# Performance work log

Hardware: AMD Instinct MI355X
Metric: run time of the kernel (lower is better)

Reference implementation:

```python
import jax, jax.numpy as jnp
import numpy as np

B, T, D = 32, 4096, 512  # D = 2 * hidden_size


def setup_inputs() -> dict:
    key = jax.random.key(0)
    k_h, k_w1, k_b1, k_w2 = jax.random.split(key, 4)
    scale = 1.0 / np.sqrt(D)
    return {
        "hidden_states": jax.random.normal(k_h, (B, T, D), dtype=jnp.float32),
        "W1": jax.random.normal(k_w1, (D, D), dtype=jnp.float32) * scale,
        "b1": jax.random.normal(k_b1, (D,), dtype=jnp.float32) * scale,
        "W2": jax.random.normal(k_w2, (D, D), dtype=jnp.float32) * scale,
    }


def reference(hidden_states, W1, b1, W2):
    # u = tanh(h @ W1^T + b1)        [B, T, D]
    u = jnp.tanh(jnp.einsum("btd,ed->bte", hidden_states, W1) + b1)
    # alphas = softmax over time axis of u @ W2^T (no bias)   [B, T, D]
    alphas = jax.nn.softmax(jnp.einsum("btd,ed->bte", u, W2), axis=1)
    # Original loop cats weighted [T, D] slices along dim 0 then sums dim 0,
    # i.e. a global reduction over batch AND time -> [D]
    return jnp.sum(hidden_states * alphas, axis=(0, 1))
```

## Files before the change

kernel.cpp:

```cpp
#include <hip/hip_runtime.h>
#include <math.h>

#define BATCH 32
#define TLEN  4096
#define DDIM  512
#define BM    128
#define BLOCK 512

typedef __attribute__((ext_vector_type(8)))  short bf16x8;
typedef __attribute__((ext_vector_type(16))) float f32x16;
typedef __attribute__((ext_vector_type(4)))  short s16x4;

__device__ __forceinline__ short f32_to_bf16_rne(float f) {
    union { float f; unsigned int u; } v; v.f = f;
    unsigned int r = (v.u + 0x7FFFu + ((v.u >> 16) & 1u)) >> 16;
    return (short)r;
}
__device__ __forceinline__ float fast_tanh(float x) {
    x = fminf(fmaxf(x, -15.f), 15.f);
    float t = __expf(2.0f * x);
    return (t - 1.0f) / (t + 1.0f);
}

__device__ __forceinline__ int lds_idx(int r, int c) {
    int g = (c >> 3) ^ (r & 31);
    return r * DDIM + (g << 3) + (c & 7);
}

__global__ void prep_kernel(const float* __restrict__ W1, const float* __restrict__ W2,
                            short* __restrict__ W1pk, short* __restrict__ W2pk,
                            float* __restrict__ lbuf, float* __restrict__ gbuf) {
    int i = blockIdx.x * blockDim.x + threadIdx.x;
    int e  = i >> 6;
    int d0 = (i & 63) << 3;
    int E = e >> 5, r = e & 31, C = d0 >> 4, half = (d0 >> 3) & 1;
    size_t src = (size_t)e * DDIM + d0;
    size_t dst = ((size_t)(E * 32 + C) * 64 + half * 32 + r) * 8;
    bf16x8 p1, p2;
    #pragma unroll
    for (int j = 0; j < 8; ++j) {
        p1[j] = f32_to_bf16_rne(W1[src + j]);
        p2[j] = f32_to_bf16_rne(W2[src + j]);
    }
    *(bf16x8*)&W1pk[dst] = p1;
    *(bf16x8*)&W2pk[dst] = p2;
    if (i < BATCH * DDIM) { lbuf[i] = 0.f; gbuf[i] = 0.f; }
}

__global__ __launch_bounds__(BLOCK, 2)
void main_kernel(const float* __restrict__ h,
                 const short* __restrict__ W1pk,
                 const float* __restrict__ b1,
                 const short* __restrict__ W2pk,
                 float* __restrict__ lbuf, float* __restrict__ gbuf) {
    __shared__ __align__(16) short sh[BM * DDIM];

    const int tid  = threadIdx.x;
    const int row0 = blockIdx.x * BM;
    const int b    = row0 / TLEN;

    {
        const float4* hp = (const float4*)(h + (size_t)row0 * DDIM);
        #pragma unroll
        for (int i = 0; i < (BM * DDIM / 4) / BLOCK; ++i) {
            int idx  = tid + i * BLOCK;
            float4 v = hp[idx];
            int flat = idx * 4;
            int r = flat >> 9;
            int c = flat & (DDIM - 1);
            s16x4 p;
            p.x = f32_to_bf16_rne(v.x); p.y = f32_to_bf16_rne(v.y);
            p.z = f32_to_bf16_rne(v.z); p.w = f32_to_bf16_rne(v.w);
            *(s16x4*)&sh[lds_idx(r, c)] = p;
        }
    }
    __syncthreads();

    const int wave = tid >> 6;
    const int lane = tid & 63;
    const int l32  = lane & 31;
    const int h5   = lane >> 5;
    const int e0   = wave * 64;

    f32x16 acc[2][4];
    #pragma unroll
    for (int i = 0; i < 2; ++i)
        #pragma unroll
        for (int j = 0; j < 4; ++j)
            #pragma unroll
            for (int r = 0; r < 16; ++r) acc[i][j][r] = 0.f;

    const short* W1p = W1pk + (size_t)(e0 >> 5) * (32 * 512) + lane * 8;
    bf16x8 wc[2][2], wn[2][2];
    #pragma unroll
    for (int eb = 0; eb < 2; ++eb)
        #pragma unroll
        for (int ks = 0; ks < 2; ++ks)
            wc[eb][ks] = *(const bf16x8*)(W1p + (eb * 32 + ks) * 512);

    #pragma unroll
    for (int i = 0; i < 16; ++i) {
        const int k0 = i * 32;
        bf16x8 hf[4][2];
        #pragma unroll
        for (int tb = 0; tb < 4; ++tb)
            #pragma unroll
            for (int ks = 0; ks < 2; ++ks)
                hf[tb][ks] = *(const bf16x8*)&sh[lds_idx(tb * 32 + l32,
                                                         k0 + ks * 16 + 8 * h5)];
        if (i < 15) {
            #pragma unroll
            for (int eb = 0; eb < 2; ++eb)
                #pragma unroll
                for (int ks = 0; ks < 2; ++ks)
                    wn[eb][ks] = *(const bf16x8*)(W1p + (eb * 32 + 2 * (i + 1) + ks) * 512);
        }
        #pragma unroll
        for (int eb = 0; eb < 2; ++eb)
            #pragma unroll
            for (int tb = 0; tb < 4; ++tb)
                #pragma unroll
                for (int ks = 0; ks < 2; ++ks)
                    acc[eb][tb] = __builtin_amdgcn_mfma_f32_32x32x16_bf16(
                        wc[eb][ks], hf[tb][ks], acc[eb][tb], 0, 0, 0);
        #pragma unroll
        for (int eb = 0; eb < 2; ++eb)
            #pragma unroll
            for (int ks = 0; ks < 2; ++ks) wc[eb][ks] = wn[eb][ks];
    }

    const short* W2p = W2pk + (size_t)(e0 >> 5) * (32 * 512) + lane * 8;
    bf16x8 w2c[2][2], w2n[2][2];
    #pragma unroll
    for (int cb = 0; cb < 2; ++cb)
        #pragma unroll
        for (int ks = 0; ks < 2; ++ks)
            w2c[cb][ks] = *(const bf16x8*)(W2p + (cb * 32 + ks) * 512);

    #pragma unroll
    for (int eb = 0; eb < 2; ++eb) {
        float4 bv[4];
        #pragma unroll
        for (int q = 0; q < 4; ++q)
            bv[q] = *(const float4*)&b1[e0 + 32 * eb + 4 * h5 + 8 * q];
        #pragma unroll
        for (int tb = 0; tb < 4; ++tb)
            #pragma unroll
            for (int r = 0; r < 16; ++r)
                acc[eb][tb][r] = fast_tanh(acc[eb][tb][r] + bv[r >> 2][r & 3]);
    }

    __syncthreads();

    #pragma unroll
    for (int eb = 0; eb < 2; ++eb)
        #pragma unroll
        for (int tb = 0; tb < 4; ++tb) {
            int tt = tb * 32 + l32;
            #pragma unroll
            for (int q = 0; q < 4; ++q) {
                int e = e0 + 32 * eb + 4 * h5 + 8 * q;
                s16x4 p;
                p.x = f32_to_bf16_rne(acc[eb][tb][4 * q + 0]);
                p.y = f32_to_bf16_rne(acc[eb][tb][4 * q + 1]);
                p.z = f32_to_bf16_rne(acc[eb][tb][4 * q + 2]);
                p.w = f32_to_bf16_rne(acc[eb][tb][4 * q + 3]);
                *(s16x4*)&sh[lds_idx(tt, e)] = p;
            }
        }
    __syncthreads();

    f32x16 acc2[4][2];
    #pragma unroll
    for (int i = 0; i < 4; ++i)
        #pragma unroll
        for (int j = 0; j < 2; ++j)
            #pragma unroll
            for (int r = 0; r < 16; ++r) acc2[i][j][r] = 0.f;

    #pragma unroll
    for (int i = 0; i < 16; ++i) {
        const int k0 = i * 32;
        bf16x8 uf[4][2];
        #pragma unroll
        for (int tb = 0; tb < 4; ++tb)
            #pragma unroll
            for (int ks = 0; ks < 2; ++ks)
                uf[tb][ks] = *(const bf16x8*)&sh[lds_idx(tb * 32 + l32,
                                                         k0 + ks * 16 + 8 * h5)];
        if (i < 15) {
            #pragma unroll
            for (int cb = 0; cb < 2; ++cb)
                #pragma unroll
                for (int ks = 0; ks < 2; ++ks)
                    w2n[cb][ks] = *(const bf16x8*)(W2p + (cb * 32 + 2 * (i + 1) + ks) * 512);
        }
        #pragma unroll
        for (int tb = 0; tb < 4; ++tb)
            #pragma unroll
            for (int cb = 0; cb < 2; ++cb)
                #pragma unroll
                for (int ks = 0; ks < 2; ++ks)
                    acc2[tb][cb] = __builtin_amdgcn_mfma_f32_32x32x16_bf16(
                        uf[tb][ks], w2c[cb][ks], acc2[tb][cb], 0, 0, 0);
        #pragma unroll
        for (int cb = 0; cb < 2; ++cb)
            #pragma unroll
            for (int ks = 0; ks < 2; ++ks) w2c[cb][ks] = w2n[cb][ks];
    }

    #pragma unroll
    for (int cb = 0; cb < 2; ++cb) {
        const int e2 = e0 + 32 * cb + l32;
        const float* hp2 = h + (size_t)row0 * DDIM + e2;
        float lsum = 0.f, gsum = 0.f;
        #pragma unroll
        for (int tb = 0; tb < 4; ++tb)
            #pragma unroll
            for (int r = 0; r < 16; ++r) {
                int tt = tb * 32 + 4 * h5 + (r & 3) + 8 * (r >> 2);
                float ev = __expf(acc2[tb][cb][r]);
                lsum += ev;
                gsum += ev * hp2[(size_t)tt * DDIM];
            }
        lsum += __shfl_xor(lsum, 32);
        gsum += __shfl_xor(gsum, 32);
        if (h5 == 0) {
            atomicAdd(&lbuf[b * DDIM + e2], lsum);
            atomicAdd(&gbuf[b * DDIM + e2], gsum);
        }
    }
}

__global__ void finish_kernel(const float* __restrict__ lbuf,
                              const float* __restrict__ gbuf,
                              float* __restrict__ out) {
    int d = blockIdx.x * blockDim.x + threadIdx.x;
    float s = 0.f;
    #pragma unroll
    for (int b = 0; b < BATCH; ++b)
        s += gbuf[b * DDIM + d] / lbuf[b * DDIM + d];
    out[d] = s;
}

extern "C" void kernel_launch(void* const* d_in, const int* in_sizes, int n_in,
                              void* d_out, int out_size, void* d_ws, size_t ws_size,
                              hipStream_t stream) {
    const float* h  = (const float*)d_in[0];
    const float* W1 = (const float*)d_in[1];
    const float* b1 = (const float*)d_in[2];
    const float* W2 = (const float*)d_in[3];
    float* out = (float*)d_out;

    char* ws = (char*)d_ws;
    short* W1pk = (short*)ws;
    short* W2pk = (short*)(ws + 512 * 1024);
    float* lbuf = (float*)(ws + 1024 * 1024);
    float* gbuf = (float*)(ws + 1024 * 1024 + 64 * 1024);

    prep_kernel<<<128, 256, 0, stream>>>(W1, W2, W1pk, W2pk, lbuf, gbuf);
    main_kernel<<<(BATCH * TLEN) / BM, BLOCK, 0, stream>>>(h, W1pk, b1, W2pk, lbuf, gbuf);
    finish_kernel<<<2, 256, 0, stream>>>(lbuf, gbuf, out);
}
```

Baseline: 563.8 us.

## Double block to 1024 threads with each wave covering 32 output columns

Each workgroup now runs 16 waves instead of 8, and each wave computes a 32-column slice of both GEMMs instead of 64. This halves per-wave accumulator and weight registers and doubles the waves per CU, since the 128KB LDS tile allows only one block per CU. The cost is that each wave reads the full h/u tile from LDS for half the MFMA work, doubling LDS read traffic per MFMA. The launch bounds now request 4 blocks per CU, which may constrain register allocation.

```diff
diff --git a/kernel.cpp b/kernel.cpp
--- a/kernel.cpp
+++ b/kernel.cpp
@@ -5,7 +5,7 @@
 #define TLEN  4096
 #define DDIM  512
 #define BM    128
-#define BLOCK 512
+#define BLOCK 1024
 
 typedef __attribute__((ext_vector_type(8)))  short bf16x8;
 typedef __attribute__((ext_vector_type(16))) float f32x16;
@@ -47,7 +47,7 @@
     if (i < BATCH * DDIM) { lbuf[i] = 0.f; gbuf[i] = 0.f; }
 }
 
-__global__ __launch_bounds__(BLOCK, 2)
+__global__ __launch_bounds__(BLOCK, 4)
 void main_kernel(const float* __restrict__ h,
                  const short* __restrict__ W1pk,
                  const float* __restrict__ b1,
@@ -80,23 +80,19 @@
     const int lane = tid & 63;
     const int l32  = lane & 31;
     const int h5   = lane >> 5;
-    const int e0   = wave * 64;
-
-    f32x16 acc[2][4];
-    #pragma unroll
-    for (int i = 0; i < 2; ++i)
-        #pragma unroll
-        for (int j = 0; j < 4; ++j)
-            #pragma unroll
-            for (int r = 0; r < 16; ++r) acc[i][j][r] = 0.f;
-
-    const short* W1p = W1pk + (size_t)(e0 >> 5) * (32 * 512) + lane * 8;
-    bf16x8 wc[2][2], wn[2][2];
-    #pragma unroll
-    for (int eb = 0; eb < 2; ++eb)
-        #pragma unroll
-        for (int ks = 0; ks < 2; ++ks)
-            wc[eb][ks] = *(const bf16x8*)(W1p + (eb * 32 + ks) * 512);
+    const int e0   = wave * 32;
+
+    f32x16 acc[4];
+    #pragma unroll
+    for (int j = 0; j < 4; ++j)
+        #pragma unroll
+        for (int r = 0; r < 16; ++r) acc[j][r] = 0.f;
+
+    const short* W1p = W1pk + (size_t)wave * (32 * 512) + lane * 8;
+    bf16x8 wc[2], wn[2];
+    #pragma unroll
+    for (int ks = 0; ks < 2; ++ks)
+        wc[ks] = *(const bf16x8*)(W1p + ks * 512);
 
     #pragma unroll
     for (int i = 0; i < 16; ++i) {
@@ -110,73 +106,60 @@
                                                          k0 + ks * 16 + 8 * h5)];
         if (i < 15) {
             #pragma unroll
-            for (int eb = 0; eb < 2; ++eb)
-                #pragma unroll
-                for (int ks = 0; ks < 2; ++ks)
-                    wn[eb][ks] = *(const bf16x8*)(W1p + (eb * 32 + 2 * (i + 1) + ks) * 512);
-        }
-        #pragma unroll
-        for (int eb = 0; eb < 2; ++eb)
-            #pragma unroll
-            for (int tb = 0; tb < 4; ++tb)
-                #pragma unroll
-                for (int ks = 0; ks < 2; ++ks)
-                    acc[eb][tb] = __builtin_amdgcn_mfma_f32_32x32x16_bf16(
-                        wc[eb][ks], hf[tb][ks], acc[eb][tb], 0, 0, 0);
-        #pragma unroll
-        for (int eb = 0; eb < 2; ++eb)
-            #pragma unroll
-            for (int ks = 0; ks < 2; ++ks) wc[eb][ks] = wn[eb][ks];
-    }
-
-    const short* W2p = W2pk + (size_t)(e0 >> 5) * (32 * 512) + lane * 8;
-    bf16x8 w2c[2][2], w2n[2][2];
-    #pragma unroll
-    for (int cb = 0; cb < 2; ++cb)
-        #pragma unroll
-        for (int ks = 0; ks < 2; ++ks)
-            w2c[cb][ks] = *(const bf16x8*)(W2p + (cb * 32 + ks) * 512);
-
-    #pragma unroll
-    for (int eb = 0; eb < 2; ++eb) {
+            for (int ks = 0; ks < 2; ++ks)
+                wn[ks] = *(const bf16x8*)(W1p + (2 * (i + 1) + ks) * 512);
+        }
+        #pragma unroll
+        for (int tb = 0; tb < 4; ++tb)
+            #pragma unroll
+            for (int ks = 0; ks < 2; ++ks)
+                acc[tb] = __builtin_amdgcn_mfma_f32_32x32x16_bf16(
+                    wc[ks], hf[tb][ks], acc[tb], 0, 0, 0);
+        #pragma unroll
+        for (int ks = 0; ks < 2; ++ks) wc[ks] = wn[ks];
+    }
+
+    const short* W2p = W2pk + (size_t)wave * (32 * 512) + lane * 8;
+    bf16x8 w2c[2], w2n[2];
+    #pragma unroll
+    for (int ks = 0; ks < 2; ++ks)
+        w2c[ks] = *(const bf16x8*)(W2p + ks * 512);
+
+    {
         float4 bv[4];
         #pragma unroll
         for (int q = 0; q < 4; ++q)
-            bv[q] = *(const float4*)&b1[e0 + 32 * eb + 4 * h5 + 8 * q];
+            bv[q] = *(const float4*)&b1[e0 + 4 * h5 + 8 * q];
         #pragma unroll
         for (int tb = 0; tb < 4; ++tb)
             #pragma unroll
             for (int r = 0; r < 16; ++r)
-                acc[eb][tb][r] = fast_tanh(acc[eb][tb][r] + bv[r >> 2][r & 3]);
+                acc[tb][r] = fast_tanh(acc[tb][r] + bv[r >> 2][r & 3]);
     }
 
     __syncthreads();
 
     #pragma unroll
-    for (int eb = 0; eb < 2; ++eb)
-        #pragma unroll
-        for (int tb = 0; tb < 4; ++tb) {
-            int tt = tb * 32 + l32;
-            #pragma unroll
-            for (int q = 0; q < 4; ++q) {
-                int e = e0 + 32 * eb + 4 * h5 + 8 * q;
-                s16x4 p;
-                p.x = f32_to_bf16_rne(acc[eb][tb][4 * q + 0]);
-                p.y = f32_to_bf16_rne(acc[eb][tb][4 * q + 1]);
-                p.z = f32_to_bf16_rne(acc[eb][tb][4 * q + 2]);
-                p.w = f32_to_bf16_rne(acc[eb][tb][4 * q + 3]);
-                *(s16x4*)&sh[lds_idx(tt, e)] = p;
-            }
-        }
+    for (int tb = 0; tb < 4; ++tb) {
+        int tt = tb * 32 + l32;
+        #pragma unroll
+        for (int q = 0; q < 4; ++q) {
+            int e = e0 + 4 * h5 + 8 * q;
+            s16x4 p;
+            p.x = f32_to_bf16_rne(acc[tb][4 * q + 0]);
+            p.y = f32_to_bf16_rne(acc[tb][4 * q + 1]);
+            p.z = f32_to_bf16_rne(acc[tb][4 * q + 2]);
+            p.w = f32_to_bf16_rne(acc[tb][4 * q + 3]);
+            *(s16x4*)&sh[lds_idx(tt, e)] = p;
+        }
+    }
     __syncthreads();
 
-    f32x16 acc2[4][2];
-    #pragma unroll
-    for (int i = 0; i < 4; ++i)
-        #pragma unroll
-        for (int j = 0; j < 2; ++j)
-            #pragma unroll
-            for (int r = 0; r < 16; ++r) acc2[i][j][r] = 0.f;
+    f32x16 acc2[4];
+    #pragma unroll
+    for (int j = 0; j < 4; ++j)
+        #pragma unroll
+        for (int r = 0; r < 16; ++r) acc2[j][r] = 0.f;
 
     #pragma unroll
     for (int i = 0; i < 16; ++i) {
@@ -190,28 +173,21 @@
                                                          k0 + ks * 16 + 8 * h5)];
         if (i < 15) {
             #pragma unroll
-            for (int cb = 0; cb < 2; ++cb)
-                #pragma unroll
-                for (int ks = 0; ks < 2; ++ks)
-                    w2n[cb][ks] = *(const bf16x8*)(W2p + (cb * 32 + 2 * (i + 1) + ks) * 512);
-        }
-        #pragma unroll
-        for (int tb = 0; tb < 4; ++tb)
-            #pragma unroll
-            for (int cb = 0; cb < 2; ++cb)
-                #pragma unroll
-                for (int ks = 0; ks < 2; ++ks)
-                    acc2[tb][cb] = __builtin_amdgcn_mfma_f32_32x32x16_bf16(
-                        uf[tb][ks], w2c[cb][ks], acc2[tb][cb], 0, 0, 0);
-        #pragma unroll
-        for (int cb = 0; cb < 2; ++cb)
-            #pragma unroll
-            for (int ks = 0; ks < 2; ++ks) w2c[cb][ks] = w2n[cb][ks];
-    }
-
-    #pragma unroll
-    for (int cb = 0; cb < 2; ++cb) {
-        const int e2 = e0 + 32 * cb + l32;
+            for (int ks = 0; ks < 2; ++ks)
+                w2n[ks] = *(const bf16x8*)(W2p + (2 * (i + 1) + ks) * 512);
+        }
+        #pragma unroll
+        for (int tb = 0; tb < 4; ++tb)
+            #pragma unroll
+            for (int ks = 0; ks < 2; ++ks)
+                acc2[tb] = __builtin_amdgcn_mfma_f32_32x32x16_bf16(
+                    uf[tb][ks], w2c[ks], acc2[tb], 0, 0, 0);
+        #pragma unroll
+        for (int ks = 0; ks < 2; ++ks) w2c[ks] = w2n[ks];
+    }
+
+    {
+        const int e2 = e0 + l32;
         const float* hp2 = h + (size_t)row0 * DDIM + e2;
         float lsum = 0.f, gsum = 0.f;
         #pragma unroll
@@ -219,7 +195,7 @@
             #pragma unroll
             for (int r = 0; r < 16; ++r) {
                 int tt = tb * 32 + 4 * h5 + (r & 3) + 8 * (r >> 2);
-                float ev = __expf(acc2[tb][cb][r]);
+                float ev = __expf(acc2[tb][r]);
                 lsum += ev;
                 gsum += ev * hp2[(size_t)tt * DDIM];
             }
```

Result: slower. 589.2 us (+4.5%).
